# Performance work log

Measured on AMD Instinct MI355X. Metric: run time of the kernel, lower is better.

## Reference

```python
import jax, jax.numpy as jnp
import numpy as np

H = 8
D = 512
DK = D // H  # 64
ALPHA = 0.2  # leaky relu negative slope


def setup_inputs() -> dict:
    key = jax.random.key(0)
    ks = jax.random.split(key, 10)
    B, N = 8, 1024
    query = jax.random.normal(ks[0], (B, N, D), dtype=jnp.float32)
    key_t = jax.random.normal(ks[1], (B, N, D), dtype=jnp.float32)
    value = jax.random.normal(ks[2], (B, N, D), dtype=jnp.float32)
    mask = jax.random.randint(ks[3], (B, N, N), 0, 2, dtype=jnp.int32)
    scale = 0.02
    Wq = jax.random.normal(ks[4], (D, D), dtype=jnp.float32) * scale
    Wk = jax.random.normal(ks[5], (D, D), dtype=jnp.float32) * scale
    Wv = jax.random.normal(ks[6], (D, D), dtype=jnp.float32) * scale
    Wo = jax.random.normal(ks[7], (D, D), dtype=jnp.float32) * scale
    bq = jnp.zeros((D,), jnp.float32)
    bk = jnp.zeros((D,), jnp.float32)
    bv = jnp.zeros((D,), jnp.float32)
    bo = jnp.zeros((D,), jnp.float32)
    # xavier-uniform-like init for the attention vector a: shape (h, 2*d_k)
    limit = float(np.sqrt(6.0 / (H + 2 * DK)))
    a = jax.random.uniform(ks[8], (H, 2 * DK), dtype=jnp.float32, minval=-limit, maxval=limit)
    return {"query": query, "key": key_t, "value": value, "mask": mask,
            "Wq": Wq, "bq": bq, "Wk": Wk, "bk": bk, "Wv": Wv, "bv": bv,
            "Wo": Wo, "bo": bo, "a": a}


def reference(query, key, value, mask, Wq, bq, Wk, bk, Wv, bv, Wo, bo, a):
    B, N, _ = query.shape

    def proj(x, W, b):
        # torch Linear: x @ W.T + b, then split heads -> (B, H, N, DK)
        return (x @ W.T + b).reshape(B, N, H, DK).transpose(0, 2, 1, 3)

    q = proj(query, Wq, bq)
    k = proj(key, Wk, bk)
    v = proj(value, Wv, bv)

    # 'cat' attention: scores[b,h,i,j] = concat(q_i, k_j) . a[h]
    #                = q_i . a[h,:DK] + k_j . a[h,DK:]  (algebraic decomposition,
    #                 avoids the O(N^2 * 2*DK) concat tensor of the torch code)
    sq = jnp.einsum('bhnd,hd->bhn', q, a[:, :DK])
    sk = jnp.einsum('bhnd,hd->bhn', k, a[:, DK:])
    scores = sq[:, :, :, None] + sk[:, :, None, :]  # (B, H, N, N)

    # mask == 0 -> -inf (mask broadcast over heads), applied BEFORE leaky relu
    scores = jnp.where(mask[:, None, :, :] == 0, -jnp.inf, scores)
    # leaky relu (leaky_relu(-inf) == -inf, preserved)
    scores = jnp.where(scores >= 0, scores, ALPHA * scores)

    p = jax.nn.softmax(scores, axis=-1)
    # fully-masked rows produce NaN -> replace with 0 (as in the torch code)
    p = jnp.where(jnp.isnan(p), jnp.zeros_like(p), p)

    x = jnp.einsum('bhnm,bhmd->bhnd', p, v)
    x = x.transpose(0, 2, 1, 3).reshape(B, N, D)
    return x @ Wo.T + bo
```

## Files before the change

kernel.cpp:

```cpp
#include <hip/hip_runtime.h>
#include <hip/hip_bf16.h>
#include <stdint.h>


typedef __attribute__((ext_vector_type(8))) short short8;
typedef __attribute__((ext_vector_type(4))) float f32x4;

#define LB __launch_bounds__(256)

union U8 { unsigned u[4]; short8 s; uint4 v; };
union U2 { unsigned u[2]; uint2 v; };

__device__ __forceinline__ unsigned short f2bf(float f) {
  unsigned int u = __float_as_uint(f);
  u += 0x7fffu + ((u >> 16) & 1u);
  return (unsigned short)(u >> 16);
}

__device__ __forceinline__ unsigned cvt_pk(float a, float b) {
  unsigned r;
  asm("v_cvt_pk_bf16_f32 %0, %1, %2" : "=v"(r) : "v"(a), "v"(b));
  return r;
}

__device__ __forceinline__ void async_cp16(const void* g, void* l) {
  __builtin_amdgcn_global_load_lds(
      (const __attribute__((address_space(1))) unsigned int*)g,
      (__attribute__((address_space(3))) unsigned int*)l, 16, 0, 0);
}

__global__ LB void prep_kernel(const float* __restrict__ Wv, const float* __restrict__ Wo,
                               unsigned short* __restrict__ wv16, unsigned short* __restrict__ wo16,
                               const float* __restrict__ Wq, const float* __restrict__ Wk,
                               const float* __restrict__ a, const float* __restrict__ bq,
                               const float* __restrict__ bk,
                               unsigned short* __restrict__ Bfrag, float* __restrict__ qkb) {
  const int blk = blockIdx.x, tid = threadIdx.x;
  if (blk < 512) {
    const float* src = blk < 256 ? Wv : Wo;
    unsigned short* dst = blk < 256 ? wv16 : wo16;
    const int idx = ((blk & 255) * 256 + tid) * 4;
    const float4 v = *(const float4*)(src + idx);
    U2 pk;
    pk.u[0] = cvt_pk(v.x, v.y);
    pk.u[1] = cvt_pk(v.z, v.w);
    *(uint2*)(dst + idx) = pk.v;
    return;
  }
  const int t = (blk - 512) * 256 + tid;
  const int d = t & 511, h = t >> 9;
  float aq = 0.f, ak = 0.f;
#pragma unroll 4
  for (int dk = 0; dk < 64; ++dk) {
    aq += Wq[(size_t)(h * 64 + dk) * 512 + d] * a[h * 128 + dk];
    ak += Wk[(size_t)(h * 64 + dk) * 512 + d] * a[h * 128 + 64 + dk];
  }
  const float L2E = 1.4426950408889634f;
  const int ks = d >> 5, lch = (d >> 3) & 3, tt = d & 7;
  Bfrag[((ks * 64 + (lch << 4) + h) << 3) + tt] = f2bf(aq * L2E);
  Bfrag[((ks * 64 + (lch << 4) + 8 + h) << 3) + tt] = f2bf(ak * L2E);
  if (d == 0) {
    float s1 = 0.f, s2 = 0.f;
    for (int dk = 0; dk < 64; ++dk) {
      s1 += bq[h * 64 + dk] * a[h * 128 + dk];
      s2 += bk[h * 64 + dk] * a[h * 128 + 64 + dk];
    }
    qkb[h] = s1 * L2E;
    qkb[8 + h] = s2 * L2E;
  }
}

__global__ LB void mid_kernel(const float* __restrict__ query, const float* __restrict__ key,
                              const unsigned short* __restrict__ Bfrag,
                              const float* __restrict__ qkb,
                              float2* __restrict__ sqE, float2* __restrict__ skE,
                              const float* __restrict__ value,
                              const unsigned short* __restrict__ wv16,
                              const float* __restrict__ bvb, unsigned short* __restrict__ vt,
                              const int* __restrict__ mask, unsigned int* __restrict__ bits) {
  __shared__ char sm[20480];
  const int tid = threadIdx.x, w = tid >> 6, l = tid & 63;
  const int lr = l & 15, lc = l >> 4;
  const int bid = blockIdx.x;
  if (bid >= 1536) {
    unsigned char* nb = (unsigned char*)sm;
    const size_t e0 = ((size_t)(bid - 1536) * 256 + tid) * 4;
    const int4 m = *(const int4*)(mask + e0);
    nb[tid] = (unsigned char)((m.x != 0) | ((m.y != 0) << 1) | ((m.z != 0) << 2) | ((m.w != 0) << 3));
    __syncthreads();
    if (tid < 32) {
      const uint2 p = *(const uint2*)(nb + tid * 8);
      const unsigned lo = p.x, hi = p.y;
      const unsigned wl = (lo & 0xFu) | ((lo >> 4) & 0xF0u) | ((lo >> 8) & 0xF00u) | ((lo >> 12) & 0xF000u);
      const unsigned wh = (hi & 0xFu) | ((hi >> 4) & 0xF0u) | ((hi >> 8) & 0xF00u) | ((hi >> 12) & 0xF000u);
      bits[(bid - 1536) * 32 + tid] = wl | (wh << 16);
    }
    return;
  }
  if (bid >= 1024) {
    float* comb = (float*)sm;
    const int m0 = (bid - 1024) * 16;
    const int k0 = w * 128;
    short8 bf[4];
#pragma unroll
    for (int ks = 0; ks < 4; ++ks)
      bf[ks] = *(const short8*)(Bfrag + (((w * 4 + ks) * 64 + l) << 3));
    const float* qbase = query + (size_t)(m0 + lr) * 512 + k0 + (lc << 3);
    const float* kbase = key + (size_t)(m0 + lr) * 512 + k0 + (lc << 3);
    f32x4 cq = {}, ck = {};
#pragma unroll
    for (int ks = 0; ks < 4; ++ks) {
      const float4 q0 = *(const float4*)(qbase + ks * 32);
      const float4 q1 = *(const float4*)(qbase + ks * 32 + 4);
      const float4 k0v = *(const float4*)(kbase + ks * 32);
      const float4 k1v = *(const float4*)(kbase + ks * 32 + 4);
      U8 aq, ak;
      aq.u[0] = cvt_pk(q0.x, q0.y); aq.u[1] = cvt_pk(q0.z, q0.w);
      aq.u[2] = cvt_pk(q1.x, q1.y); aq.u[3] = cvt_pk(q1.z, q1.w);
      ak.u[0] = cvt_pk(k0v.x, k0v.y); ak.u[1] = cvt_pk(k0v.z, k0v.w);
      ak.u[2] = cvt_pk(k1v.x, k1v.y); ak.u[3] = cvt_pk(k1v.z, k1v.w);
      cq = __builtin_amdgcn_mfma_f32_16x16x32_bf16(aq.s, bf[ks], cq, 0, 0, 0);
      ck = __builtin_amdgcn_mfma_f32_16x16x32_bf16(ak.s, bf[ks], ck, 0, 0, 0);
    }
    if (w) {
      float* p = comb + ((w - 1) * 64 + l) * 9;
#pragma unroll
      for (int r = 0; r < 4; ++r) { p[r] = cq[r]; p[4 + r] = ck[r]; }
    }
    __syncthreads();
    if (w == 0) {
#pragma unroll
      for (int j = 0; j < 3; ++j) {
        const float* p = comb + (j * 64 + l) * 9;
#pragma unroll
        for (int r = 0; r < 4; ++r) { cq[r] += p[r]; ck[r] += p[4 + r]; }
      }
      const int col = l & 15;
      const int mbase = m0 + (lc << 2);
      const int b = mbase >> 10;
      const float bia = qkb[col];
      if (col < 8) {
        float2* out = sqE + ((size_t)b * 8 + col) * 1024;
#pragma unroll
        for (int r = 0; r < 4; ++r) {
          const float v = cq[r] + bia;
          float2 pr;
          pr.x = __builtin_amdgcn_exp2f(v);
          pr.y = __builtin_amdgcn_exp2f(0.2f * v);
          out[(mbase + r) & 1023] = pr;
        }
      } else {
        float2* out = skE + ((size_t)b * 8 + (col - 8)) * 1024;
#pragma unroll
        for (int r = 0; r < 4; ++r) {
          const float v = ck[r] + bia;
          float2 pr;
          pr.x = __builtin_amdgcn_exp2f(v);
          pr.y = __builtin_amdgcn_exp2f(0.2f * v);
          out[(mbase + r) & 1023] = pr;
        }
      }
    }
    return;
  }
  unsigned short* As = (unsigned short*)sm;
  unsigned short* Bs = (unsigned short*)(sm + 4096);
  const int bm = bid >> 2, bn = bid & 3;
  const int m0 = bm * 32, n0 = bn * 128;
  const int wr = (w & 1) * 16, wc = (w >> 1) * 64;
  const int rch = (lc ^ ((lr >> 1) & 3)) << 3;
  const int arow = (w << 3) + (l >> 3);
  const int akc = l & 7;
  const float* asrc = value + (size_t)(m0 + arow) * 512 + (akc << 2);
  const int ach = ((akc >> 1) ^ ((arow >> 1) & 3));
  const int aoff = arow * 32 + (ach << 3) + ((akc & 1) << 2);
  const int crow = l >> 2;
  const int brow0 = (w << 4) + crow, brow1 = ((w + 4) << 4) + crow;
  const unsigned short* bsrc0 = wv16 + (size_t)(n0 + brow0) * 512 + (((l & 3) ^ ((brow0 >> 1) & 3)) << 3);
  const unsigned short* bsrc1 = wv16 + (size_t)(n0 + brow1) * 512 + (((l & 3) ^ ((brow1 >> 1) & 3)) << 3);

  f32x4 acc[4] = {};
  float4 areg = *(const float4*)(asrc);
  async_cp16(bsrc0, Bs + (w << 9));
  async_cp16(bsrc1, Bs + ((w + 4) << 9));
  {
    U2 aw;
    aw.u[0] = cvt_pk(areg.x, areg.y);
    aw.u[1] = cvt_pk(areg.z, areg.w);
    *(uint2*)(As + aoff) = aw.v;
  }
  areg = *(const float4*)(asrc + 32);
  async_cp16(bsrc0 + 32, Bs + 4096 + (w << 9));
  async_cp16(bsrc1 + 32, Bs + 4096 + ((w + 4) << 9));
  asm volatile("s_waitcnt vmcnt(3)" ::: "memory");
  asm volatile("s_waitcnt lgkmcnt(0)" ::: "memory");
  __builtin_amdgcn_sched_barrier(0);
  __builtin_amdgcn_s_barrier();
  int buf = 0;
  for (int kt = 0; kt < 16; ++kt) {
    const short8 af = *(const short8*)(As + (buf << 10) + (wr + lr) * 32 + rch);
    __builtin_amdgcn_s_setprio(1);
#pragma unroll
    for (int j = 0; j < 4; ++j) {
      const short8 bfr = *(const short8*)(Bs + (buf << 12) + (wc + j * 16 + lr) * 32 + rch);
      acc[j] = __builtin_amdgcn_mfma_f32_16x16x32_bf16(af, bfr, acc[j], 0, 0, 0);
    }
    __builtin_amdgcn_s_setprio(0);
    __builtin_amdgcn_s_barrier();
    if (kt < 15) {
      U2 aw;
      aw.u[0] = cvt_pk(areg.x, areg.y);
      aw.u[1] = cvt_pk(areg.z, areg.w);
      *(uint2*)(As + ((buf ^ 1) << 10) + aoff) = aw.v;
      if (kt < 14) {
        areg = *(const float4*)(asrc + (kt + 2) * 32);
        async_cp16(bsrc0 + (kt + 2) * 32, Bs + (buf << 12) + (w << 9));
        async_cp16(bsrc1 + (kt + 2) * 32, Bs + (buf << 12) + ((w + 4) << 9));
        asm volatile("s_waitcnt vmcnt(3)" ::: "memory");
      } else {
        asm volatile("s_waitcnt vmcnt(0)" ::: "memory");
      }
      asm volatile("s_waitcnt lgkmcnt(0)" ::: "memory");
      __builtin_amdgcn_sched_barrier(0);
      __builtin_amdgcn_s_barrier();
    }
    buf ^= 1;
  }
#pragma unroll
  for (int j = 0; j < 4; ++j) {
    const int nn = n0 + wc + j * 16 + lr;
    const float bia = bvb[nn];
    const int mm0 = m0 + wr + lc * 4;
    const int b = mm0 >> 10, t0 = mm0 & 1023;
    const int h = nn >> 6, dk = nn & 63;
    U2 pk;
    pk.u[0] = cvt_pk(acc[j][0] + bia, acc[j][1] + bia);
    pk.u[1] = cvt_pk(acc[j][2] + bia, acc[j][3] + bia);
    *(uint2*)(vt + (((size_t)((b * 8 + h) * 64 + dk)) << 10) + t0) = pk.v;
  }
}

template <int BB16>
__global__ LB void gemm_bt(const unsigned short* __restrict__ A,
                           const void* __restrict__ Bwp,
                           const float* __restrict__ bias, float* __restrict__ outp) {
  __shared__ unsigned short As[2][32 * 32];
  __shared__ unsigned short Bs[2][128 * 32];
  const int tid = threadIdx.x;
  const int w = tid >> 6, l = tid & 63;
  const int lr = l & 15, lc = l >> 4;
  const int bm = blockIdx.x >> 2, bn = blockIdx.x & 3;
  const int m0 = bm * 32, n0 = bn * 128;
  const int wr = (w & 1) * 16, wc = (w >> 1) * 64;
  const int rch = (lc ^ ((lr >> 1) & 3)) << 3;
  const int arow = (w << 3) + (l >> 2);
  const int asc = (l & 3) ^ ((arow >> 1) & 3);
  const unsigned short* asrc = A + (size_t)(m0 + arow) * 512 + (asc << 3);
  const int crow = l >> 2;
  const unsigned short* b16 = (const unsigned short*)Bwp;
  const float* b32 = (const float*)Bwp;
  const int brow0 = (w << 4) + crow, brow1 = ((w + 4) << 4) + crow;
  const unsigned short* bsrc0 = b16 + (size_t)(n0 + brow0) * 512 + (((l & 3) ^ ((brow0 >> 1) & 3)) << 3);
  const unsigned short* bsrc1 = b16 + (size_t)(n0 + brow1) * 512 + (((l & 3) ^ ((brow1 >> 1) & 3)) << 3);

  f32x4 acc[4] = {};
  if (BB16) {
    if (l < 32) async_cp16(asrc, As[0] + (w << 8));
    async_cp16(bsrc0, Bs[0] + (w << 9));
    async_cp16(bsrc1, Bs[0] + ((w + 4) << 9));
    int buf = 0;
    for (int kt = 0; kt < 16; ++kt) {
      if (kt < 15) {
        const int k1 = (kt + 1) * 32;
        if (l < 32) async_cp16(asrc + k1, As[buf ^ 1] + (w << 8));
        async_cp16(bsrc0 + k1, Bs[buf ^ 1] + (w << 9));
        async_cp16(bsrc1 + k1, Bs[buf ^ 1] + ((w + 4) << 9));
        asm volatile("s_waitcnt vmcnt(3)" ::: "memory");
      } else {
        asm volatile("s_waitcnt vmcnt(0)" ::: "memory");
      }
      __builtin_amdgcn_sched_barrier(0);
      __builtin_amdgcn_s_barrier();
      const short8 af = *(const short8*)(As[buf] + (wr + lr) * 32 + rch);
      __builtin_amdgcn_s_setprio(1);
#pragma unroll
      for (int j = 0; j < 4; ++j) {
        const short8 bfr = *(const short8*)(Bs[buf] + (wc + j * 16 + lr) * 32 + rch);
        acc[j] = __builtin_amdgcn_mfma_f32_16x16x32_bf16(af, bfr, acc[j], 0, 0, 0);
      }
      __builtin_amdgcn_s_setprio(0);
      if (kt < 15) __builtin_amdgcn_s_barrier();
      buf ^= 1;
    }
  } else {
    for (int kt = 0; kt < 16; ++kt) {
      const int k0 = kt * 32;
      if (kt) __syncthreads();
      if (l < 32) async_cp16(asrc + k0, As[0] + (w << 8));
#pragma unroll
      for (int it = 0; it < 2; ++it) {
        const int idx = it * 256 + tid;
        const int row = idx >> 2, gr = idx & 3;
        const int sch = (gr ^ ((row >> 1) & 3)) << 3;
        const float4* src = (const float4*)(b32 + (size_t)(n0 + row) * 512 + k0 + gr * 8);
        const float4 b0 = src[0], b1 = src[1];
        U8 t8;
        t8.u[0] = cvt_pk(b0.x, b0.y); t8.u[1] = cvt_pk(b0.z, b0.w);
        t8.u[2] = cvt_pk(b1.x, b1.y); t8.u[3] = cvt_pk(b1.z, b1.w);
        *(uint4*)(Bs[0] + row * 32 + sch) = t8.v;
      }
      __syncthreads();
      const short8 af = *(const short8*)(As[0] + (wr + lr) * 32 + rch);
#pragma unroll
      for (int j = 0; j < 4; ++j) {
        const short8 bfr = *(const short8*)(Bs[0] + (wc + j * 16 + lr) * 32 + rch);
        acc[j] = __builtin_amdgcn_mfma_f32_16x16x32_bf16(af, bfr, acc[j], 0, 0, 0);
      }
    }
  }
#pragma unroll
  for (int j = 0; j < 4; ++j) {
    const int nn = n0 + wc + j * 16 + lr;
    const float bia = bias[nn];
    const int mm0 = m0 + wr + lc * 4;
#pragma unroll
    for (int r = 0; r < 4; ++r)
      outp[(size_t)(mm0 + r) * 512 + nn] = acc[j][r] + bia;
  }
}

__global__ LB void attn_kernel(const float2* __restrict__ sqE, const float2* __restrict__ skE,
                               const unsigned char* __restrict__ mbits,
                               const unsigned short* __restrict__ vt,
                               unsigned short* __restrict__ xb) {
  __shared__ char smem[24576];
  float* sksE = (float*)smem;
  char* mks = smem + 8192;
  const int tid = threadIdx.x;
  const int w = tid >> 6, l = tid & 63;
  const int lr = l & 15, lc = l >> 4;
  const int bid = blockIdx.x;
  const int bh = bid & 63, iblk = bid >> 6;
  const int b = bh >> 3, h = bh & 7;
  const int i0b = iblk << 7;
  const int rh = w & 1, jh = w >> 1;
  const int j0 = jh << 9;
  const float* sqEp = (const float*)(sqE + (size_t)bh * 1024);
  const float* skEp = (const float*)(skE + (size_t)bh * 1024);
  const unsigned short* vtp = vt + ((size_t)bh << 16);
  const unsigned char* mrow = mbits + ((size_t)b << 17);

  async_cp16(skEp + (w << 9) + l * 4, sksE + (w << 9));
  async_cp16(skEp + (w << 9) + 256 + l * 4, sksE + (w << 9) + 256);
#pragma unroll
  for (int m = 0; m < 4; ++m) {
    const int row = (w << 5) + (m << 3) + (l >> 3);
    const int c = (l & 7) ^ (row & 7);
    async_cp16(mrow + (size_t)(i0b + row) * 128 + (c << 4), mks + (w << 12) + (m << 10));
  }
  float2 E8[4];
#pragma unroll
  for (int t = 0; t < 4; ++t)
    E8[t] = *(const float2*)(sqEp + ((i0b + (rh << 6) + (t << 4) + lr) << 1));
  __syncthreads();

  f32x4 acc[4][4] = {};
  f32x4 accs[4] = {};
  short8 ones;
#pragma unroll
  for (int t = 0; t < 8; ++t) ones[t] = (short)0x3f80;
  const int rx = (lr & 7) << 4;

  const unsigned short* vfr = vtp + (size_t)lr * 1024 + j0 + (lc << 3);
  short8 bvc[4], bvn[4];
#pragma unroll
  for (int c = 0; c < 4; ++c)
    bvc[c] = *(const short8*)(vfr + (c << 14));

  for (int it = 0; it < 16; ++it) {
    const int jb = j0 + (it << 5);
    const int qb = (jb >> 3) + lc;
    const float* sp = sksE + ((jb + (lc << 3)) << 1);
    const f32x4 q0 = *(const f32x4*)(sp);
    const f32x4 q1 = *(const f32x4*)(sp + 4);
    const f32x4 q2 = *(const f32x4*)(sp + 8);
    const f32x4 q3 = *(const f32x4*)(sp + 12);
    if (it < 15) {
#pragma unroll
      for (int c = 0; c < 4; ++c)
        bvn[c] = *(const short8*)(vfr + ((it + 1) << 5) + (c << 14));
    }
    U8 pa[4];
#pragma unroll
    for (int t = 0; t < 4; ++t) {
      const int row = (rh << 6) + (t << 4) + lr;
      const unsigned mb = (unsigned char)mks[(row << 7) + (qb ^ rx)];
      const float Eq = E8[t].x, eq = E8[t].y;
      float e[8];
      e[0] = fmaxf(Eq * q0[0], eq * q0[1]); e[1] = fmaxf(Eq * q0[2], eq * q0[3]);
      e[2] = fmaxf(Eq * q1[0], eq * q1[1]); e[3] = fmaxf(Eq * q1[2], eq * q1[3]);
      e[4] = fmaxf(Eq * q2[0], eq * q2[1]); e[5] = fmaxf(Eq * q2[2], eq * q2[3]);
      e[6] = fmaxf(Eq * q3[0], eq * q3[1]); e[7] = fmaxf(Eq * q3[2], eq * q3[3]);
#pragma unroll
      for (int u = 0; u < 8; ++u)
        e[u] = (mb & (1u << u)) ? e[u] : 0.0f;
      pa[t].u[0] = cvt_pk(e[0], e[1]); pa[t].u[1] = cvt_pk(e[2], e[3]);
      pa[t].u[2] = cvt_pk(e[4], e[5]); pa[t].u[3] = cvt_pk(e[6], e[7]);
    }
    __builtin_amdgcn_s_setprio(1);
#pragma unroll
    for (int c = 0; c < 4; ++c)
#pragma unroll
      for (int t = 0; t < 4; ++t)
        acc[t][c] = __builtin_amdgcn_mfma_f32_16x16x32_bf16(pa[t].s, bvc[c], acc[t][c], 0, 0, 0);
#pragma unroll
    for (int t = 0; t < 4; ++t)
      accs[t] = __builtin_amdgcn_mfma_f32_16x16x32_bf16(pa[t].s, ones, accs[t], 0, 0, 0);
    __builtin_amdgcn_s_setprio(0);
#pragma unroll
    for (int c = 0; c < 4; ++c) bvc[c] = bvn[c];
  }

  float* cmb = (float*)smem;
  __syncthreads();
#pragma unroll 1
  for (int rr = 0; rr < 2; ++rr) {
    if (jh == 1 && rh == rr) {
      float* p = cmb + l * 81;
#pragma unroll
      for (int t = 0; t < 4; ++t) {
#pragma unroll
        for (int c = 0; c < 4; ++c) *(f32x4*)(p + (t * 4 + c) * 4) = acc[t][c];
        *(f32x4*)(p + 64 + t * 4) = accs[t];
      }
    }
    __syncthreads();
    if (jh == 0 && rh == rr) {
      const float* p = cmb + l * 81;
#pragma unroll
      for (int t = 0; t < 4; ++t) {
#pragma unroll
        for (int c = 0; c < 4; ++c) {
          const f32x4 v = *(const f32x4*)(p + (t * 4 + c) * 4);
#pragma unroll
          for (int r = 0; r < 4; ++r) acc[t][c][r] += v[r];
        }
        const f32x4 vs = *(const f32x4*)(p + 64 + t * 4);
#pragma unroll
        for (int r = 0; r < 4; ++r) accs[t][r] += vs[r];
      }
#pragma unroll
      for (int t = 0; t < 4; ++t) {
#pragma unroll
        for (int r = 0; r < 4; ++r) {
          const float sv = accs[t][r];
          const float inv = sv > 0.0f ? 1.0f / sv : 0.0f;
          const int i = i0b + (rh << 6) + (t << 4) + (lc << 2) + r;
#pragma unroll
          for (int c = 0; c < 4; ++c)
            xb[(((size_t)(b * 1024 + i)) << 9) + h * 64 + (c << 4) + lr] =
                f2bf(acc[t][c][r] * inv);
        }
      }
    }
    __syncthreads();
  }
}

extern "C" void kernel_launch(void* const* d_in, const int* in_sizes, int n_in,
                              void* d_out, int out_size, void* d_ws, size_t ws_size,
                              hipStream_t stream) {
  const float* query = (const float*)d_in[0];
  const float* key   = (const float*)d_in[1];
  const float* value = (const float*)d_in[2];
  const int*   mask  = (const int*)d_in[3];
  const float* Wq = (const float*)d_in[4];
  const float* bq = (const float*)d_in[5];
  const float* Wk = (const float*)d_in[6];
  const float* bk = (const float*)d_in[7];
  const float* Wv = (const float*)d_in[8];
  const float* bv = (const float*)d_in[9];
  const float* Wo = (const float*)d_in[10];
  const float* bo = (const float*)d_in[11];
  const float* a  = (const float*)d_in[12];

  char* oc = (char*)d_out;
  unsigned short* vt = (unsigned short*)(oc + 0);
  unsigned int* mbits = (unsigned int*)(oc + 8388608);
  unsigned short* Bfrag = (unsigned short*)(oc + 9961472);
  float* qkb = (float*)(oc + 9977856);
  unsigned short* wv16 = (unsigned short*)(oc + 10485760);
  float2* sqE = (float2*)(oc + 11010048);
  float2* skE = (float2*)(oc + 11534336);
  unsigned short* wo16f = (unsigned short*)(oc + 12058624);
  unsigned short* xb = (unsigned short*)d_ws;

  const bool roomy = ws_size >= 8912896;
  unsigned short* wo16 = roomy ? (unsigned short*)((char*)d_ws + 8388608) : wo16f;

  prep_kernel<<<528, 256, 0, stream>>>(Wv, Wo, wv16, wo16, Wq, Wk, a, bq, bk, Bfrag, qkb);
  mid_kernel<<<9728, 256, 0, stream>>>(query, key, Bfrag, qkb, sqE, skE,
                                       value, wv16, bv, vt, mask, mbits);
  attn_kernel<<<512, 256, 0, stream>>>(sqE, skE, (const unsigned char*)mbits, vt, xb);
  if (roomy)
    gemm_bt<1><<<1024, 256, 0, stream>>>(xb, (const void*)wo16, bo, (float*)d_out);
  else
    gemm_bt<0><<<1024, 256, 0, stream>>>(xb, (const void*)Wo, bo, (float*)d_out);
}
```

Measured before the change: 78.73 us.

## Split attention key dimension across four waves with 64-row blocks, doubling grid

The attention kernel now gives each block 64 query rows instead of 128, and each of the four waves covers a quarter of the key range (256 keys) instead of half-rows by half-keys. This doubles the grid to 1024 blocks for better occupancy and load balance on the many-CU device. Partial results are combined through a three-step shared-memory reduction into wave 0. The main loop is fully unrolled and drops the explicit V register double buffering, leaving load scheduling to the compiler. In exchange the reduction has more serialized steps and each key tile is reused across fewer query rows.

```diff
diff --git a/kernel.cpp b/kernel.cpp
--- a/kernel.cpp
+++ b/kernel.cpp
@@ -333,7 +333,7 @@
                                const unsigned char* __restrict__ mbits,
                                const unsigned short* __restrict__ vt,
                                unsigned short* __restrict__ xb) {
-  __shared__ char smem[24576];
+  __shared__ char smem[21504];
   float* sksE = (float*)smem;
   char* mks = smem + 8192;
   const int tid = threadIdx.x;
@@ -342,9 +342,8 @@
   const int bid = blockIdx.x;
   const int bh = bid & 63, iblk = bid >> 6;
   const int b = bh >> 3, h = bh & 7;
-  const int i0b = iblk << 7;
-  const int rh = w & 1, jh = w >> 1;
-  const int j0 = jh << 9;
+  const int i0b = iblk << 6;
+  const int j0 = w << 8;
   const float* sqEp = (const float*)(sqE + (size_t)bh * 1024);
   const float* skEp = (const float*)(skE + (size_t)bh * 1024);
   const unsigned short* vtp = vt + ((size_t)bh << 16);
@@ -353,15 +352,15 @@
   async_cp16(skEp + (w << 9) + l * 4, sksE + (w << 9));
   async_cp16(skEp + (w << 9) + 256 + l * 4, sksE + (w << 9) + 256);
 #pragma unroll
-  for (int m = 0; m < 4; ++m) {
-    const int row = (w << 5) + (m << 3) + (l >> 3);
+  for (int m = 0; m < 2; ++m) {
+    const int row = (w << 4) + (m << 3) + (l >> 3);
     const int c = (l & 7) ^ (row & 7);
-    async_cp16(mrow + (size_t)(i0b + row) * 128 + (c << 4), mks + (w << 12) + (m << 10));
+    async_cp16(mrow + (size_t)(i0b + row) * 128 + (c << 4), mks + (w << 11) + (m << 10));
   }
   float2 E8[4];
 #pragma unroll
   for (int t = 0; t < 4; ++t)
-    E8[t] = *(const float2*)(sqEp + ((i0b + (rh << 6) + (t << 4) + lr) << 1));
+    E8[t] = *(const float2*)(sqEp + ((i0b + (t << 4) + lr) << 1));
   __syncthreads();
 
   f32x4 acc[4][4] = {};
@@ -372,28 +371,24 @@
   const int rx = (lr & 7) << 4;
 
   const unsigned short* vfr = vtp + (size_t)lr * 1024 + j0 + (lc << 3);
-  short8 bvc[4], bvn[4];
-#pragma unroll
-  for (int c = 0; c < 4; ++c)
-    bvc[c] = *(const short8*)(vfr + (c << 14));
-
-  for (int it = 0; it < 16; ++it) {
-    const int jb = j0 + (it << 5);
+
+#pragma unroll
+  for (int s = 0; s < 8; ++s) {
+    const int jb = j0 + (s << 5);
     const int qb = (jb >> 3) + lc;
     const float* sp = sksE + ((jb + (lc << 3)) << 1);
     const f32x4 q0 = *(const f32x4*)(sp);
     const f32x4 q1 = *(const f32x4*)(sp + 4);
     const f32x4 q2 = *(const f32x4*)(sp + 8);
     const f32x4 q3 = *(const f32x4*)(sp + 12);
-    if (it < 15) {
-#pragma unroll
-      for (int c = 0; c < 4; ++c)
-        bvn[c] = *(const short8*)(vfr + ((it + 1) << 5) + (c << 14));
-    }
+    short8 bv[4];
+#pragma unroll
+    for (int c = 0; c < 4; ++c)
+      bv[c] = *(const short8*)(vfr + (s << 5) + (c << 14));
     U8 pa[4];
 #pragma unroll
     for (int t = 0; t < 4; ++t) {
-      const int row = (rh << 6) + (t << 4) + lr;
+      const int row = (t << 4) + lr;
       const unsigned mb = (unsigned char)mks[(row << 7) + (qb ^ rx)];
       const float Eq = E8[t].x, eq = E8[t].y;
       float e[8];
@@ -412,20 +407,18 @@
     for (int c = 0; c < 4; ++c)
 #pragma unroll
       for (int t = 0; t < 4; ++t)
-        acc[t][c] = __builtin_amdgcn_mfma_f32_16x16x32_bf16(pa[t].s, bvc[c], acc[t][c], 0, 0, 0);
+        acc[t][c] = __builtin_amdgcn_mfma_f32_16x16x32_bf16(pa[t].s, bv[c], acc[t][c], 0, 0, 0);
 #pragma unroll
     for (int t = 0; t < 4; ++t)
       accs[t] = __builtin_amdgcn_mfma_f32_16x16x32_bf16(pa[t].s, ones, accs[t], 0, 0, 0);
     __builtin_amdgcn_s_setprio(0);
-#pragma unroll
-    for (int c = 0; c < 4; ++c) bvc[c] = bvn[c];
   }
 
   float* cmb = (float*)smem;
   __syncthreads();
 #pragma unroll 1
-  for (int rr = 0; rr < 2; ++rr) {
-    if (jh == 1 && rh == rr) {
+  for (int src = 1; src < 4; ++src) {
+    if (w == src) {
       float* p = cmb + l * 81;
 #pragma unroll
       for (int t = 0; t < 4; ++t) {
@@ -435,7 +428,7 @@
       }
     }
     __syncthreads();
-    if (jh == 0 && rh == rr) {
+    if (w == 0) {
       const float* p = cmb + l * 81;
 #pragma unroll
       for (int t = 0; t < 4; ++t) {
@@ -449,21 +442,23 @@
 #pragma unroll
         for (int r = 0; r < 4; ++r) accs[t][r] += vs[r];
       }
-#pragma unroll
-      for (int t = 0; t < 4; ++t) {
-#pragma unroll
-        for (int r = 0; r < 4; ++r) {
-          const float sv = accs[t][r];
-          const float inv = sv > 0.0f ? 1.0f / sv : 0.0f;
-          const int i = i0b + (rh << 6) + (t << 4) + (lc << 2) + r;
-#pragma unroll
-          for (int c = 0; c < 4; ++c)
-            xb[(((size_t)(b * 1024 + i)) << 9) + h * 64 + (c << 4) + lr] =
-                f2bf(acc[t][c][r] * inv);
-        }
-      }
     }
     __syncthreads();
+  }
+  if (w == 0) {
+#pragma unroll
+    for (int t = 0; t < 4; ++t) {
+#pragma unroll
+      for (int r = 0; r < 4; ++r) {
+        const float sv = accs[t][r];
+        const float inv = sv > 0.0f ? 1.0f / sv : 0.0f;
+        const int i = i0b + (t << 4) + (lc << 2) + r;
+#pragma unroll
+        for (int c = 0; c < 4; ++c)
+          xb[(((size_t)(b * 1024 + i)) << 9) + h * 64 + (c << 4) + lr] =
+              f2bf(acc[t][c][r] * inv);
+      }
+    }
   }
 }
 
@@ -501,7 +496,7 @@
   prep_kernel<<<528, 256, 0, stream>>>(Wv, Wo, wv16, wo16, Wq, Wk, a, bq, bk, Bfrag, qkb);
   mid_kernel<<<9728, 256, 0, stream>>>(query, key, Bfrag, qkb, sqE, skE,
                                        value, wv16, bv, vt, mask, mbits);
-  attn_kernel<<<512, 256, 0, stream>>>(sqE, skE, (const unsigned char*)mbits, vt, xb);
+  attn_kernel<<<1024, 256, 0, stream>>>(sqE, skE, (const unsigned char*)mbits, vt, xb);
   if (roomy)
     gemm_bt<1><<<1024, 256, 0, stream>>>(xb, (const void*)wo16, bo, (float*)d_out);
   else
```

Measured after the change: 85.41 us. 8.5% more time.
